# Kernel optimization log

Hardware: AMD Instinct MI355X
Metric: run time of the kernel (lower is better)

The kernel has to match this reference:

```python
import jax, jax.numpy as jnp
import numpy as np

E = 256       # embed_size
H2 = 2 * E    # feature / encoder-output dim
B = 128
S = 512
OUT = 256


def setup_inputs() -> dict:
    key = jax.random.key(0)
    ks = jax.random.split(key, 20)
    p = lambda k, shp: (jax.random.normal(k, shp, jnp.float32) * 0.05)
    return {
        "inputs": jax.random.normal(ks[0], (B, S, H2), jnp.float32),
        # encoder BiLSTM (input 2E, hidden E), pytorch gate order i,f,g,o
        "enc_Wih_f": p(ks[1], (4 * E, H2)), "enc_Whh_f": p(ks[2], (4 * E, E)),
        "enc_bih_f": p(ks[3], (4 * E,)),    "enc_bhh_f": p(ks[4], (4 * E,)),
        "enc_Wih_b": p(ks[5], (4 * E, H2)), "enc_Whh_b": p(ks[6], (4 * E, E)),
        "enc_bih_b": p(ks[7], (4 * E,)),    "enc_bhh_b": p(ks[8], (4 * E,)),
        # decoder LSTM (input 2E, hidden 2E); called with zero state each step,
        # so W_hh and the forget gate contribute exactly zero -> omitted.
        "dec_Wih": p(ks[9], (4 * H2, H2)),
        "dec_bih": p(ks[10], (4 * H2,)), "dec_bhh": p(ks[11], (4 * H2,)),
        # attention + output head
        "attW": p(ks[12], (H2, H2)), "attW_b": p(ks[13], (H2,)),
        "attU": p(ks[14], (1, H2)),  "attU_b": p(ks[15], (1,)),
        "outW": p(ks[16], (OUT, H2)), "outW_b": p(ks[17], (OUT,)),
    }


def _lstm_dir(x, Wih, Whh, bih, bhh, reverse):
    """Single-direction LSTM, zero init state. x: (B,S,D) -> (B,S,E)."""
    pre = jnp.einsum("bsd,gd->bsg", x, Wih) + bih + bhh  # (B,S,4E)
    Eh = Whh.shape[1]

    def step(carry, p):
        h, c = carry
        g = p + h @ Whh.T
        i, f, gg, o = jnp.split(g, 4, axis=-1)
        c = jax.nn.sigmoid(f) * c + jax.nn.sigmoid(i) * jnp.tanh(gg)
        h = jax.nn.sigmoid(o) * jnp.tanh(c)
        return (h, c), h

    bsz = x.shape[0]
    init = (jnp.zeros((bsz, Eh), x.dtype), jnp.zeros((bsz, Eh), x.dtype))
    _, hs = jax.lax.scan(step, init, jnp.swapaxes(pre, 0, 1), reverse=reverse)
    return jnp.swapaxes(hs, 0, 1)


def _dec_cell(x, Wih, bih, bhh):
    """One LSTM step with zero (h,c): forget term and h@Whh vanish."""
    g = x @ Wih.T + bih + bhh
    i, _f, gg, o = jnp.split(g, 4, axis=-1)
    c = jax.nn.sigmoid(i) * jnp.tanh(gg)
    return jax.nn.sigmoid(o) * jnp.tanh(c)


def reference(inputs, enc_Wih_f, enc_Whh_f, enc_bih_f, enc_bhh_f,
              enc_Wih_b, enc_Whh_b, enc_bih_b, enc_bhh_b,
              dec_Wih, dec_bih, dec_bhh,
              attW, attW_b, attU, attU_b, outW, outW_b):
    bsz, seq, _ = inputs.shape
    # BiLSTM encoder
    hf = _lstm_dir(inputs, enc_Wih_f, enc_Whh_f, enc_bih_f, enc_bhh_f, False)
    hb = _lstm_dir(inputs, enc_Wih_b, enc_Whh_b, enc_bih_b, enc_bhh_b, True)
    enc = jnp.concatenate([hf, hb], axis=-1)  # (B,S,2E)

    # per-step decoder: each torch call re-zeros the LSTM state; input chains
    x0 = enc[:, -1, :]  # (B,2E)

    def dstep(h, _):
        h = _dec_cell(h, dec_Wih, dec_bih, dec_bhh)
        return h, h

    _, dec_ys = jax.lax.scan(dstep, x0, None, length=seq)
    dec_out = jnp.swapaxes(dec_ys, 0, 1)  # (B,S,2E)

    ae_loss = jnp.mean((inputs - jax.lax.stop_gradient(dec_out)) ** 2)

    # attention pooling (softmax over size-1 axis -> all-ones, as in original)
    enc2 = inputs + enc
    att = jnp.tanh(enc2 @ attW.T + attW_b)
    w = jax.nn.softmax(att @ attU.T + attU_b, axis=2)      # (B,S,1)
    pooled = jnp.einsum("bsd,bso->bod", enc2, w)           # (B,1,2E)
    outputs = pooled @ outW.T + outW_b                      # (B,1,OUT)
    return outputs.reshape(bsz, 1, 1, OUT), ae_loss
```

## Files before the change

### kernel.cpp

```cpp
#include <hip/hip_runtime.h>
#include <hip/hip_bf16.h>
#include <hip/hip_fp16.h>
#include <stdint.h>

#define B_ 128
#define S_ 512
#define E_ 256
#define H2_ 512
#define G_ 1024
#define DG_ 2048
#define M_ (B_*S_)

typedef float f32x4 __attribute__((ext_vector_type(4)));
typedef short s16x8 __attribute__((ext_vector_type(8)));
typedef _Float16 h16x2 __attribute__((ext_vector_type(2)));

__device__ __forceinline__ float sigm(float x){ return 1.f/(1.f+__expf(-x)); }
__device__ __forceinline__ float tanh_f(float x){ return 1.f - 2.f/(__expf(2.f*x)+1.f); }

__device__ __forceinline__ void gload_lds16(const void* g, void* l){
  __builtin_amdgcn_global_load_lds(
      (const __attribute__((address_space(1))) void*)g,
      (__attribute__((address_space(3))) void*)l,
      16, 0, 0);
}

__device__ __forceinline__ uint32_t enc_e4m3(float f){
  uint32_t u = __float_as_uint(f);
  uint32_t s = (u >> 24) & 0x80u;
  float af = fabsf(f);
  if (!(af > 0.f)) return s;
  if (af >= 448.f) return s | 0x7Eu;
  int ex = (int)((u >> 23) & 0xFF) - 127;
  uint32_t man = u & 0x7FFFFFu;
  int bexp = ex + 7;
  if (bexp <= 0){
    uint32_t qi = (uint32_t)rintf(af * 512.f);
    if (qi > 8u) qi = 8u;
    return s | qi;
  }
  uint32_t keep = man >> 20;
  uint32_t rest = man & 0xFFFFFu;
  const uint32_t half = 0x80000u;
  if (rest > half || (rest == half && (keep & 1u))) keep++;
  if (keep == 8u){ keep = 0u; bexp++; }
  if (bexp >= 16) return s | 0x7Eu;
  if (bexp == 15 && keep == 7u) keep = 6u;
  return s | ((uint32_t)bexp << 3) | keep;
}

__device__ __forceinline__ uint32_t f32_to_fp8_byte(float v){
#if __has_builtin(__builtin_amdgcn_cvt_pk_fp8_f32)
  int pk = __builtin_amdgcn_cvt_pk_fp8_f32(v, v, 0, false);
  return (uint32_t)pk & 0xFFu;
#else
  return enc_e4m3(v);
#endif
}

__device__ __forceinline__ float dot2_f16(uint32_t a, uint32_t b, float acc){
#if __has_builtin(__builtin_amdgcn_fdot2)
  return __builtin_amdgcn_fdot2(__builtin_bit_cast(h16x2,a), __builtin_bit_cast(h16x2,b), acc, false);
#else
  __half2 ah = __builtin_bit_cast(__half2, a), bh = __builtin_bit_cast(__half2, b);
  float2 af = __half22float2(ah), bf = __half22float2(bh);
  return fmaf(af.x, bf.x, fmaf(af.y, bf.y, acc));
#endif
}

__global__ __launch_bounds__(512) void k_prep_enc(
    const float* __restrict__ wf, const float* __restrict__ wb,
    const float* __restrict__ bihf, const float* __restrict__ bhhf,
    const float* __restrict__ bihb, const float* __restrict__ bhhb,
    ushort* __restrict__ Wenc, float* __restrict__ bsum){
  int n = blockIdx.x, d = threadIdx.x;
  const float* src = (n < G_) ? (wf + (size_t)n*H2_) : (wb + (size_t)(n-G_)*H2_);
  __hip_bfloat16 h = __float2bfloat16(src[d]);
  Wenc[(size_t)n*H2_ + d] = __builtin_bit_cast(ushort, h);
  if (d == 0) bsum[n] = (n < G_) ? (bihf[n] + bhhf[n]) : (bihb[n-G_] + bhhb[n-G_]);
}

__global__ __launch_bounds__(64) void k_prep_whh_pk(
    const float* __restrict__ whf, const float* __restrict__ whb, uint8_t* __restrict__ Wp){
  int bid = blockIdx.x;
  int lane = threadIdx.x;
  int d   = bid >> 8;
  int rem = bid & 255;
  int wid = rem >> 5;
  int tl  = (rem >> 2) & 7;
  int p   = rem & 3;
  int gt = tl & 3, uh = tl >> 2;
  const float* src = d ? whb : whf;
  int row = gt*256 + wid*32 + uh*16 + (lane & 15);
  int hk  = (lane >> 4) * 8;
  uint8_t bytes[16];
  #pragma unroll
  for (int e = 0; e < 8; ++e){
    bytes[e]     = (uint8_t)enc_e4m3(src[(size_t)row*E_ + (2*p)*32   + hk + e]);
    bytes[8 + e] = (uint8_t)enc_e4m3(src[(size_t)row*E_ + (2*p+1)*32 + hk + e]);
  }
  uint8_t* dst = Wp + ((size_t)bid)*1024 + lane*16;
  *(uint4*)dst = *(const uint4*)bytes;
}

__global__ __launch_bounds__(64) void k_prep_dec(
    const float* __restrict__ wd, const float* __restrict__ bih, const float* __restrict__ bhh,
    uint4* __restrict__ wdt, float* __restrict__ bsumd){
  int row = blockIdx.x, u = threadIdx.x;
  const float* src = wd + (size_t)row*H2_ + u*8;
  union { _Float16 h[8]; uint4 q; } pk;
  #pragma unroll
  for (int i=0;i<8;i++) pk.h[i] = (_Float16)src[i];
  wdt[(size_t)u*DG_ + row] = pk.q;
  if (u == 0) bsumd[row] = bih[row] + bhh[row];
}

__global__ __launch_bounds__(512) void k_xstat(
    const float* __restrict__ X, float* __restrict__ SX, float* __restrict__ SX2){
  int b = blockIdx.x, d = threadIdx.x;
  const float* xb = X + (size_t)b*S_*H2_;
  float s=0.f, s2=0.f;
  for (int t=0;t<S_;++t){ float v = xb[(size_t)t*H2_ + d]; s += v; s2 = fmaf(v,v,s2); }
  SX[(size_t)b*H2_+d]=s; SX2[(size_t)b*H2_+d]=s2;
}

__global__ __launch_bounds__(256) void k_gemm_pre_t(
    const float* __restrict__ X, const ushort* __restrict__ Wenc,
    const float* __restrict__ bsum, ushort* __restrict__ preT){
  __shared__ __align__(16) ushort smem[128*130];
  ushort (*As)[64] = (ushort (*)[64])(smem);
  ushort (*Bs)[64] = (ushort (*)[64])(smem + 8192);
  int n0 = blockIdx.x * 128;
  int tt = blockIdx.y;
  int tid = threadIdx.x, lane = tid & 63, wq = tid >> 6;
  int wr = wq >> 1, wc = wq & 1;
  f32x4 acc[4][4] = {};
  for (int kt=0; kt<8; ++kt){
    int k0 = kt*64;
    #pragma unroll
    for (int it=0; it<4; ++it){
      int slot = tid + it*256;
      int r = slot >> 3, c8 = (slot & 7)*8;
      const float* ap = X + ((size_t)(r*512 + tt))*512 + k0 + c8;
      float4 a0 = *(const float4*)ap;
      float4 a1 = *(const float4*)(ap+4);
      union { __hip_bfloat16 h[8]; uint4 q; } pk;
      pk.h[0]=__float2bfloat16(a0.x); pk.h[1]=__float2bfloat16(a0.y);
      pk.h[2]=__float2bfloat16(a0.z); pk.h[3]=__float2bfloat16(a0.w);
      pk.h[4]=__float2bfloat16(a1.x); pk.h[5]=__float2bfloat16(a1.y);
      pk.h[6]=__float2bfloat16(a1.z); pk.h[7]=__float2bfloat16(a1.w);
      *(uint4*)&As[r][c8] = pk.q;
      *(uint4*)&Bs[r][c8] = *(const uint4*)(Wenc + (size_t)(n0+r)*512 + k0 + c8);
    }
    __syncthreads();
    #pragma unroll
    for (int kk=0; kk<2; ++kk){
      int krow = kk*32 + (lane>>4)*8;
      s16x8 af[4], bf[4];
      #pragma unroll
      for (int mi=0;mi<4;mi++) af[mi] = *(const s16x8*)&As[wr*64+mi*16+(lane&15)][krow];
      #pragma unroll
      for (int ni=0;ni<4;ni++) bf[ni] = *(const s16x8*)&Bs[wc*64+ni*16+(lane&15)][krow];
      #pragma unroll
      for (int mi=0;mi<4;mi++){
        #pragma unroll
        for (int ni=0;ni<4;ni++)
          acc[mi][ni] = __builtin_amdgcn_mfma_f32_16x16x32_bf16(af[mi], bf[ni], acc[mi][ni], 0,0,0);
      }
    }
    __syncthreads();
  }
  #pragma unroll
  for (int ni=0; ni<4; ++ni){
    int n_l = wc*64 + ni*16 + (lane&15);
    float bs = bsum[n0 + n_l];
    #pragma unroll
    for (int mi=0; mi<4; ++mi){
      int bb = wr*64 + mi*16 + (lane>>4)*4;
      #pragma unroll
      for (int r2=0;r2<4;r2++){
        __hip_bfloat16 hv = __float2bfloat16(acc[mi][ni][r2] + bs);
        smem[n_l*130 + bb + r2] = __builtin_bit_cast(ushort, hv);
      }
    }
  }
  __syncthreads();
  #pragma unroll
  for (int it=0; it<64; ++it){
    int n_l = it*2 + (tid>>7);
    int b = tid & 127;
    preT[(((size_t)tt*8 + (b>>4))*2048 + n0 + n_l)*16 + (b & 15)] = smem[n_l*130 + b];
  }
}

__global__ __launch_bounds__(512) void k_enc_mfma(
    const ushort* __restrict__ preT, const uint8_t* __restrict__ Wp,
    float* __restrict__ SH, float* __restrict__ x0){
  int wg = blockIdx.x;
  int dir = wg >> 3;
  int b0q = wg & 7;
  int b0 = b0q * 16;
  int t = threadIdx.x, lane = t & 63, wid = t >> 6;
  __shared__ __align__(16) uint4  wlds[8*14*64];
  __shared__ __align__(16) ushort pbuf[2048*8];
  __shared__ __align__(16) uint8_t hb[2][16*264];

  {
    const uint4* src = (const uint4*)(Wp + ((size_t)(dir*8 + wid))*32768);
    #pragma unroll
    for (int c=0; c<14; ++c)
      wlds[(wid*14 + c)*64 + lane] = src[c*64 + lane];
  }
  for (int i=t; i<2*16*264; i+=512) ((uint8_t*)hb)[i] = 0;

  int frow = lane & 15;
  int mb = (lane >> 4) * 4;
  int u0 = wid*32 + frow;
  float c_st[8] = {0,0,0,0,0,0,0,0};
  float sumh[8] = {0,0,0,0,0,0,0,0};
  const uint4* wp0 = (const uint4*)(Wp + ((size_t)(dir*8 + wid))*32768);
  __syncthreads();

  int pb = 0;
  for (int s=0; s<S_; ++s){
    int ts = dir ? (S_-1-s) : s;
    {
      const uint8_t* gb = (const uint8_t*)(preT + (((size_t)ts*8 + b0q)*2048 + (size_t)dir*1024)*16);
      uint8_t* lb = (uint8_t*)pbuf;
      #pragma unroll
      for (int c=0; c<4; ++c){
        gload_lds16(gb + (((wid*4 + c)*64 + lane) << 4), lb + (wid*4 + c)*1024);
      }
    }
    long long a_ll[8];
    {
      const uint8_t* ar = &hb[pb][frow*264 + ((lane>>4)*8)];
      #pragma unroll
      for (int kk=0; kk<8; ++kk){
        uint2 v = *(const uint2*)(ar + kk*32);
        a_ll[kk] = (((long long)v.y) << 32) | (unsigned int)v.x;
      }
    }
    const uint4* wl = wp0;
    const uint4* wl2 = &wlds[(wid*14)*64 + lane];
    asm volatile("" : "+v"(wl), "+v"(wl2));
    f32x4 acc[8] = {};
    #pragma unroll
    for (int tl=0; tl<8; ++tl){
      #pragma unroll
      for (int p=0; p<4; ++p){
        int c = tl*4 + p;
        uint4 q = (c < 14) ? wl2[c*64] : wl[c*64 + lane];
        long long bf0 = (((long long)q.y) << 32) | (unsigned int)q.x;
        long long bf1 = (((long long)q.w) << 32) | (unsigned int)q.z;
        acc[tl] = __builtin_amdgcn_mfma_f32_16x16x32_fp8_fp8(a_ll[2*p],   bf0, acc[tl], 0,0,0);
        acc[tl] = __builtin_amdgcn_mfma_f32_16x16x32_fp8_fp8(a_ll[2*p+1], bf1, acc[tl], 0,0,0);
      }
    }
    __syncthreads();
    int wx0 = (dir==0 && s==S_-1) || (dir==1 && s==0);
    #pragma unroll
    for (int uh=0; uh<2; ++uh){
      int r0 = u0 + uh*16;
      uint2 pvv[4];
      #pragma unroll
      for (int gt=0; gt<4; ++gt)
        pvv[gt] = *(const uint2*)&pbuf[(gt*256 + r0)*16 + mb];
      #pragma unroll
      for (int r=0; r<4; ++r){
        int si = uh*4 + r;
        unsigned w0 = (r < 2) ? pvv[0].x : pvv[0].y;
        unsigned w1 = (r < 2) ? pvv[1].x : pvv[1].y;
        unsigned w2 = (r < 2) ? pvv[2].x : pvv[2].y;
        unsigned w3 = (r < 2) ? pvv[3].x : pvv[3].y;
        unsigned sh16 = (r & 1) ? 16u : 0u;
        float gi = acc[uh*4+0][r] + __uint_as_float(((w0 >> sh16) & 0xFFFFu) << 16);
        float gf = acc[uh*4+1][r] + __uint_as_float(((w1 >> sh16) & 0xFFFFu) << 16);
        float gg = acc[uh*4+2][r] + __uint_as_float(((w2 >> sh16) & 0xFFFFu) << 16);
        float go = acc[uh*4+3][r] + __uint_as_float(((w3 >> sh16) & 0xFFFFu) << 16);
        float cn = sigm(gf)*c_st[si] + sigm(gi)*tanh_f(gg);
        float hn = sigm(go)*tanh_f(cn);
        c_st[si] = cn;
        sumh[si] += hn;
        hb[pb^1][(mb+r)*264 + r0] = (uint8_t)f32_to_fp8_byte(hn);
        if (wx0) x0[(size_t)(b0+mb+r)*H2_ + dir*E_ + r0] = hn;
      }
    }
    __syncthreads();
    pb ^= 1;
  }
  #pragma unroll
  for (int uh=0; uh<2; ++uh)
    #pragma unroll
    for (int r=0; r<4; ++r)
      SH[((size_t)dir*B_ + b0 + mb + r)*E_ + u0 + uh*16] = sumh[uh*4+r];
}

#define EPS_CONV 2e-6f
__global__ __launch_bounds__(512) void k_dec(
    const float* __restrict__ X, const uint4* __restrict__ wdt,
    const float* __restrict__ bsumd, const float* __restrict__ x0,
    const float* __restrict__ SX, const float* __restrict__ SX2,
    float* __restrict__ loss_b){
  int b = blockIdx.x, j = threadIdx.x;
  __shared__ _Float16 hl[512];
  __shared__ float red[512];
  float h = x0[(size_t)b*H2_ + j];
  hl[j] = (_Float16)h;
  float bi = bsumd[j], bg = bsumd[j+1024], bo = bsumd[j+1536];
  float sxp = 0.f, x2p = 0.f, lacc = 0.f;
  const float* xb = X + (size_t)b*S_*H2_;
  int done = S_;
  __syncthreads();
  for (int s=0; s<S_; ++s){
    float ai = bi, ag = bg, ao = bo;
    const uint4* hp = (const uint4*)hl;
    const uint4* wi = wdt + j;
    const uint4* wgp = wdt + j + 1024;
    const uint4* wo = wdt + j + 1536;
    #pragma unroll 8
    for (int u=0; u<64; ++u){
      uint4 hv = hp[u];
      uint4 a = wi[(size_t)u*DG_];
      uint4 g = wgp[(size_t)u*DG_];
      uint4 o = wo[(size_t)u*DG_];
      ai = dot2_f16(a.x, hv.x, ai); ai = dot2_f16(a.y, hv.y, ai);
      ai = dot2_f16(a.z, hv.z, ai); ai = dot2_f16(a.w, hv.w, ai);
      ag = dot2_f16(g.x, hv.x, ag); ag = dot2_f16(g.y, hv.y, ag);
      ag = dot2_f16(g.z, hv.z, ag); ag = dot2_f16(g.w, hv.w, ag);
      ao = dot2_f16(o.x, hv.x, ao); ao = dot2_f16(o.y, hv.y, ao);
      ao = dot2_f16(o.z, hv.z, ao); ao = dot2_f16(o.w, hv.w, ao);
    }
    float cc = sigm(ai) * tanh_f(ag);
    float hn = sigm(ao) * tanh_f(cc);
    float xv = xb[(size_t)s*H2_ + j];
    float dd = xv - hn;
    lacc += dd*dd; sxp += xv; x2p = fmaf(xv,xv,x2p);
    float delta = fabsf(hn - h);
    h = hn;
    __syncthreads();
    hl[j] = (_Float16)h;
    if (__syncthreads_count(delta > EPS_CONV) == 0){ done = s+1; break; }
  }
  if (done < S_){
    size_t o = (size_t)b*H2_ + j;
    float rx = SX[o] - sxp, rx2 = SX2[o] - x2p;
    float rem = (float)(S_ - done);
    lacc += rx2 - 2.f*h*rx + rem*h*h;
  }
  red[j] = lacc;
  __syncthreads();
  for (int st=256; st>0; st>>=1){
    if (j < st) red[j] += red[j+st];
    __syncthreads();
  }
  if (j == 0) loss_b[b] = red[0];
}

__global__ __launch_bounds__(256) void k_out(
    const float* __restrict__ SX, const float* __restrict__ SH,
    const float* __restrict__ outW, const float* __restrict__ outWb,
    const float* __restrict__ loss_b, float* __restrict__ out){
  int b = blockIdx.x, o = threadIdx.x;
  __shared__ float pooled[512];
  for (int d=o; d<512; d+=256){
    float v = SX[(size_t)b*H2_ + d];
    v += (d < E_) ? SH[(size_t)b*E_ + d] : SH[(size_t)(B_ + b)*E_ + (d - E_)];
    pooled[d] = v;
  }
  __syncthreads();
  const float4* w4 = (const float4*)(outW + (size_t)o*H2_);
  const float4* p4 = (const float4*)pooled;
  float acc = outWb[o];
  #pragma unroll 16
  for (int i=0;i<128;i++){
    float4 w = w4[i], p = p4[i];
    acc = fmaf(w.x,p.x,acc); acc = fmaf(w.y,p.y,acc);
    acc = fmaf(w.z,p.z,acc); acc = fmaf(w.w,p.w,acc);
  }
  out[(size_t)b*256 + o] = acc;
  if (b == 0 && o == 0){
    float L = 0.f;
    for (int i=0;i<B_;i++) L += loss_b[i];
    out[32768] = L / 33554432.f;
  }
}

extern "C" void kernel_launch(void* const* d_in, const int* in_sizes, int n_in,
                              void* d_out, int out_size, void* d_ws, size_t ws_size,
                              hipStream_t stream) {
  const float* X     = (const float*)d_in[0];
  const float* Wihf  = (const float*)d_in[1];
  const float* Whhf  = (const float*)d_in[2];
  const float* bihf  = (const float*)d_in[3];
  const float* bhhf  = (const float*)d_in[4];
  const float* Wihb  = (const float*)d_in[5];
  const float* Whhb  = (const float*)d_in[6];
  const float* bihb  = (const float*)d_in[7];
  const float* bhhb  = (const float*)d_in[8];
  const float* Wdec  = (const float*)d_in[9];
  const float* dbih  = (const float*)d_in[10];
  const float* dbhh  = (const float*)d_in[11];
  const float* outW  = (const float*)d_in[16];
  const float* outWb = (const float*)d_in[17];
  float* out = (float*)d_out;

  char* ws = (char*)d_ws;
  size_t off = 0;
  auto alloc = [&](size_t bytes){ void* p = ws + off; off += (bytes + 255) & ~(size_t)255; return p; };
  ushort* preT         = (ushort*)alloc((size_t)S_*DG_*B_*2);
  ushort* Wenc         = (ushort*)alloc((size_t)DG_*H2_*2);
  float* bsum          = (float*)alloc((size_t)DG_*4);
  uint8_t* Wp          = (uint8_t*)alloc((size_t)2*G_*E_);
  uint4* wdt           = (uint4*)alloc((size_t)64*DG_*16);
  float* bsumd         = (float*)alloc((size_t)DG_*4);
  float* SX            = (float*)alloc((size_t)B_*H2_*4);
  float* SX2           = (float*)alloc((size_t)B_*H2_*4);
  float* SH            = (float*)alloc((size_t)2*B_*E_*4);
  float* x0            = (float*)alloc((size_t)B_*H2_*4);
  float* loss_b        = (float*)alloc((size_t)B_*4);

  hipLaunchKernelGGL(k_prep_enc, dim3(DG_), dim3(512), 0, stream,
                     Wihf, Wihb, bihf, bhhf, bihb, bhhb, Wenc, bsum);
  hipLaunchKernelGGL(k_prep_whh_pk, dim3(512), dim3(64), 0, stream, Whhf, Whhb, Wp);
  hipLaunchKernelGGL(k_prep_dec, dim3(DG_), dim3(64), 0, stream, Wdec, dbih, dbhh, wdt, bsumd);
  hipLaunchKernelGGL(k_xstat, dim3(B_), dim3(H2_), 0, stream, X, SX, SX2);
  hipLaunchKernelGGL(k_gemm_pre_t, dim3(16, 512), dim3(256), 0, stream, X, Wenc, bsum, preT);
  hipLaunchKernelGGL(k_enc_mfma, dim3(16), dim3(512), 0, stream, preT, Wp, SH, x0);
  hipLaunchKernelGGL(k_dec, dim3(B_), dim3(512), 0, stream, X, wdt, bsumd, x0, SX, SX2, loss_b);
  hipLaunchKernelGGL(k_out, dim3(B_), dim3(256), 0, stream, SX, SH, outW, outWb, loss_b, out);
}
```

Measured before the change: 3.691 ms.

## Split encoder recurrence across 16 waves per block instead of 8

The recurrent encoder kernel now runs 1024 threads (16 waves) per block, each wave owning 16 hidden units instead of 32. This halves the per-wave MFMA chain and gate-activation work on the serial per-timestep critical path. The Whh packing kernel is relaid out to match, and the LDS weight cache per wave shrinks to 7 chunks. The costs are more waves contending at each per-step barrier and more global weight loads per step, since the LDS-cached fraction falls.

```diff
diff --git a/kernel.cpp b/kernel.cpp
--- a/kernel.cpp
+++ b/kernel.cpp
@@ -86,12 +86,11 @@
   int lane = threadIdx.x;
   int d   = bid >> 8;
   int rem = bid & 255;
-  int wid = rem >> 5;
-  int tl  = (rem >> 2) & 7;
+  int wid = rem >> 4;
+  int gt  = (rem >> 2) & 3;
   int p   = rem & 3;
-  int gt = tl & 3, uh = tl >> 2;
   const float* src = d ? whb : whf;
-  int row = gt*256 + wid*32 + uh*16 + (lane & 15);
+  int row = gt*256 + wid*16 + (lane & 15);
   int hk  = (lane >> 4) * 8;
   uint8_t bytes[16];
   #pragma unroll
@@ -193,7 +192,7 @@
   }
 }
 
-__global__ __launch_bounds__(512) void k_enc_mfma(
+__global__ __launch_bounds__(1024) void k_enc_mfma(
     const ushort* __restrict__ preT, const uint8_t* __restrict__ Wp,
     float* __restrict__ SH, float* __restrict__ x0){
   int wg = blockIdx.x;
@@ -201,24 +200,21 @@
   int b0q = wg & 7;
   int b0 = b0q * 16;
   int t = threadIdx.x, lane = t & 63, wid = t >> 6;
-  __shared__ __align__(16) uint4  wlds[8*14*64];
+  __shared__ __align__(16) uint4  wlds[16*7*64];
   __shared__ __align__(16) ushort pbuf[2048*8];
   __shared__ __align__(16) uint8_t hb[2][16*264];
 
-  {
-    const uint4* src = (const uint4*)(Wp + ((size_t)(dir*8 + wid))*32768);
-    #pragma unroll
-    for (int c=0; c<14; ++c)
-      wlds[(wid*14 + c)*64 + lane] = src[c*64 + lane];
-  }
-  for (int i=t; i<2*16*264; i+=512) ((uint8_t*)hb)[i] = 0;
+  const uint4* wp0 = (const uint4*)(Wp + ((size_t)(dir*16 + wid))*16384);
+  #pragma unroll
+  for (int c=0; c<7; ++c)
+    wlds[(wid*7 + c)*64 + lane] = wp0[c*64 + lane];
+  for (int i=t; i<2*16*264; i+=1024) ((uint8_t*)hb)[i] = 0;
 
   int frow = lane & 15;
   int mb = (lane >> 4) * 4;
-  int u0 = wid*32 + frow;
-  float c_st[8] = {0,0,0,0,0,0,0,0};
-  float sumh[8] = {0,0,0,0,0,0,0,0};
-  const uint4* wp0 = (const uint4*)(Wp + ((size_t)(dir*8 + wid))*32768);
+  int u0 = wid*16 + frow;
+  float c_st[4] = {0,0,0,0};
+  float sumh[4] = {0,0,0,0};
   __syncthreads();
 
   int pb = 0;
@@ -228,9 +224,8 @@
       const uint8_t* gb = (const uint8_t*)(preT + (((size_t)ts*8 + b0q)*2048 + (size_t)dir*1024)*16);
       uint8_t* lb = (uint8_t*)pbuf;
       #pragma unroll
-      for (int c=0; c<4; ++c){
-        gload_lds16(gb + (((wid*4 + c)*64 + lane) << 4), lb + (wid*4 + c)*1024);
-      }
+      for (int c=0; c<2; ++c)
+        gload_lds16(gb + (((wid*2 + c)*64 + lane) << 4), lb + (wid*2 + c)*1024);
     }
     long long a_ll[8];
     {
@@ -242,58 +237,51 @@
       }
     }
     const uint4* wl = wp0;
-    const uint4* wl2 = &wlds[(wid*14)*64 + lane];
+    const uint4* wl2 = &wlds[(wid*7)*64 + lane];
     asm volatile("" : "+v"(wl), "+v"(wl2));
-    f32x4 acc[8] = {};
-    #pragma unroll
-    for (int tl=0; tl<8; ++tl){
+    f32x4 acc[4] = {};
+    #pragma unroll
+    for (int gt=0; gt<4; ++gt){
       #pragma unroll
       for (int p=0; p<4; ++p){
-        int c = tl*4 + p;
-        uint4 q = (c < 14) ? wl2[c*64] : wl[c*64 + lane];
+        int c = gt*4 + p;
+        uint4 q = (c < 7) ? wl2[c*64] : wl[c*64 + lane];
         long long bf0 = (((long long)q.y) << 32) | (unsigned int)q.x;
         long long bf1 = (((long long)q.w) << 32) | (unsigned int)q.z;
-        acc[tl] = __builtin_amdgcn_mfma_f32_16x16x32_fp8_fp8(a_ll[2*p],   bf0, acc[tl], 0,0,0);
-        acc[tl] = __builtin_amdgcn_mfma_f32_16x16x32_fp8_fp8(a_ll[2*p+1], bf1, acc[tl], 0,0,0);
+        acc[gt] = __builtin_amdgcn_mfma_f32_16x16x32_fp8_fp8(a_ll[2*p],   bf0, acc[gt], 0,0,0);
+        acc[gt] = __builtin_amdgcn_mfma_f32_16x16x32_fp8_fp8(a_ll[2*p+1], bf1, acc[gt], 0,0,0);
       }
     }
     __syncthreads();
     int wx0 = (dir==0 && s==S_-1) || (dir==1 && s==0);
-    #pragma unroll
-    for (int uh=0; uh<2; ++uh){
-      int r0 = u0 + uh*16;
-      uint2 pvv[4];
-      #pragma unroll
-      for (int gt=0; gt<4; ++gt)
-        pvv[gt] = *(const uint2*)&pbuf[(gt*256 + r0)*16 + mb];
-      #pragma unroll
-      for (int r=0; r<4; ++r){
-        int si = uh*4 + r;
-        unsigned w0 = (r < 2) ? pvv[0].x : pvv[0].y;
-        unsigned w1 = (r < 2) ? pvv[1].x : pvv[1].y;
-        unsigned w2 = (r < 2) ? pvv[2].x : pvv[2].y;
-        unsigned w3 = (r < 2) ? pvv[3].x : pvv[3].y;
-        unsigned sh16 = (r & 1) ? 16u : 0u;
-        float gi = acc[uh*4+0][r] + __uint_as_float(((w0 >> sh16) & 0xFFFFu) << 16);
-        float gf = acc[uh*4+1][r] + __uint_as_float(((w1 >> sh16) & 0xFFFFu) << 16);
-        float gg = acc[uh*4+2][r] + __uint_as_float(((w2 >> sh16) & 0xFFFFu) << 16);
-        float go = acc[uh*4+3][r] + __uint_as_float(((w3 >> sh16) & 0xFFFFu) << 16);
-        float cn = sigm(gf)*c_st[si] + sigm(gi)*tanh_f(gg);
-        float hn = sigm(go)*tanh_f(cn);
-        c_st[si] = cn;
-        sumh[si] += hn;
-        hb[pb^1][(mb+r)*264 + r0] = (uint8_t)f32_to_fp8_byte(hn);
-        if (wx0) x0[(size_t)(b0+mb+r)*H2_ + dir*E_ + r0] = hn;
-      }
+    uint2 pvv[4];
+    #pragma unroll
+    for (int gt=0; gt<4; ++gt)
+      pvv[gt] = *(const uint2*)&pbuf[(gt*256 + u0)*16 + mb];
+    #pragma unroll
+    for (int r=0; r<4; ++r){
+      unsigned w0 = (r < 2) ? pvv[0].x : pvv[0].y;
+      unsigned w1 = (r < 2) ? pvv[1].x : pvv[1].y;
+      unsigned w2 = (r < 2) ? pvv[2].x : pvv[2].y;
+      unsigned w3 = (r < 2) ? pvv[3].x : pvv[3].y;
+      unsigned sh16 = (r & 1) ? 16u : 0u;
+      float gi = acc[0][r] + __uint_as_float(((w0 >> sh16) & 0xFFFFu) << 16);
+      float gf = acc[1][r] + __uint_as_float(((w1 >> sh16) & 0xFFFFu) << 16);
+      float gg = acc[2][r] + __uint_as_float(((w2 >> sh16) & 0xFFFFu) << 16);
+      float go = acc[3][r] + __uint_as_float(((w3 >> sh16) & 0xFFFFu) << 16);
+      float cn = sigm(gf)*c_st[r] + sigm(gi)*tanh_f(gg);
+      float hn = sigm(go)*tanh_f(cn);
+      c_st[r] = cn;
+      sumh[r] += hn;
+      hb[pb^1][(mb+r)*264 + u0] = (uint8_t)f32_to_fp8_byte(hn);
+      if (wx0) x0[(size_t)(b0+mb+r)*H2_ + dir*E_ + u0] = hn;
     }
     __syncthreads();
     pb ^= 1;
   }
   #pragma unroll
-  for (int uh=0; uh<2; ++uh)
-    #pragma unroll
-    for (int r=0; r<4; ++r)
-      SH[((size_t)dir*B_ + b0 + mb + r)*E_ + u0 + uh*16] = sumh[uh*4+r];
+  for (int r=0; r<4; ++r)
+    SH[((size_t)dir*B_ + b0 + mb + r)*E_ + u0] = sumh[r];
 }
 
 #define EPS_CONV 2e-6f
@@ -426,7 +414,7 @@
   hipLaunchKernelGGL(k_prep_dec, dim3(DG_), dim3(64), 0, stream, Wdec, dbih, dbhh, wdt, bsumd);
   hipLaunchKernelGGL(k_xstat, dim3(B_), dim3(H2_), 0, stream, X, SX, SX2);
   hipLaunchKernelGGL(k_gemm_pre_t, dim3(16, 512), dim3(256), 0, stream, X, Wenc, bsum, preT);
-  hipLaunchKernelGGL(k_enc_mfma, dim3(16), dim3(512), 0, stream, preT, Wp, SH, x0);
+  hipLaunchKernelGGL(k_enc_mfma, dim3(16), dim3(1024), 0, stream, preT, Wp, SH, x0);
   hipLaunchKernelGGL(k_dec, dim3(B_), dim3(512), 0, stream, X, wdt, bsumd, x0, SX, SX2, loss_b);
   hipLaunchKernelGGL(k_out, dim3(B_), dim3(256), 0, stream, SX, SH, outW, outWb, loss_b, out);
 }
```

Result: faster. 3.423 ms (-7.3%).
